# Optimization experiments

Hardware: AMD Instinct MI355X
Metric: run time of the kernel (lower is better)

## Reference

```python
import jax, jax.numpy as jnp
import numpy as np

D_MODEL = 768
N_LAYER = 4
VOCAB = 50280
D_STATE = 16
D_INNER = 1536
DT_RANK = 48
D_CONV = 4
BATCH = 2
SEQ = 1024
EPS = 1e-5


def setup_inputs() -> dict:
    key = jax.random.key(0)
    ks = jax.random.split(key, 8)
    s = 0.02
    A_log = jnp.broadcast_to(
        jnp.log(jnp.arange(1, D_STATE + 1, dtype=jnp.float32)),
        (N_LAYER, D_INNER, D_STATE)).copy()
    return {
        "input_ids": jax.random.randint(ks[0], (BATCH, SEQ), 0, VOCAB, dtype=jnp.int32),
        "embedding": jax.random.normal(ks[1], (VOCAB, D_MODEL)) * s,
        "in_proj_w": jax.random.normal(ks[2], (N_LAYER, D_MODEL, 2 * D_INNER)) * s,
        "conv_w": jax.random.normal(ks[3], (N_LAYER, D_INNER, D_CONV)) * s,
        "conv_b": jnp.zeros((N_LAYER, D_INNER)),
        "x_proj_w": jax.random.normal(ks[4], (N_LAYER, D_INNER, DT_RANK + 2 * D_STATE)) * s,
        "dt_proj_w": jax.random.normal(ks[5], (N_LAYER, DT_RANK, D_INNER)) * s,
        "dt_proj_b": jnp.zeros((N_LAYER, D_INNER)),
        "A_log": A_log,
        "D": jnp.ones((N_LAYER, D_INNER)),
        "out_proj_w": jax.random.normal(ks[6], (N_LAYER, D_INNER, D_MODEL)) * s,
        "norm_w": jnp.ones((N_LAYER, D_MODEL)),
        "norm_f_w": jnp.ones((D_MODEL,)),
    }


def rmsnorm(x, w):
    return x * jax.lax.rsqrt(jnp.mean(x * x, axis=-1, keepdims=True) + EPS) * w


def depthwise_causal_conv(x, w, b):
    # x: [b, l, d_in], w: [d_in, k] depthwise kernel, causal left padding (k-1)
    k = w.shape[-1]
    y = jax.lax.conv_general_dilated(
        x.transpose(0, 2, 1), w[:, None, :], window_strides=(1,),
        padding=[(k - 1, 0)], feature_group_count=w.shape[0],
        dimension_numbers=('NCH', 'OIH', 'NCH'))
    return y.transpose(0, 2, 1) + b


def selective_scan(u, delta, A, Bm, Cm, Dv):
    # u, delta: [b,l,d]; A: [d,n]; Bm,Cm: [b,l,n]; Dv: [d]
    deltaA = jnp.exp(delta[..., None] * A)                          # [b,l,d,n]
    deltaB_u = delta[..., None] * Bm[:, :, None, :] * u[..., None]  # [b,l,d,n]

    def step(x, inp):
        a_t, bu_t, c_t = inp            # [b,d,n], [b,d,n], [b,n]
        x = a_t * x + bu_t
        y = jnp.einsum('bdn,bn->bd', x, c_t)
        return x, y

    x0 = jnp.zeros((u.shape[0], u.shape[2], A.shape[1]), u.dtype)
    _, ys = jax.lax.scan(step, x0, (deltaA.transpose(1, 0, 2, 3),
                                    deltaB_u.transpose(1, 0, 2, 3),
                                    Cm.transpose(1, 0, 2)))
    return ys.transpose(1, 0, 2) + u * Dv


def mamba_block(x, in_w, cw, cb, xw, dtw, dtb, alog, d, ow):
    xr = x @ in_w                                   # [b,l,2*d_inner]
    xs, res = jnp.split(xr, 2, axis=-1)
    xs = jax.nn.silu(depthwise_causal_conv(xs, cw, cb))
    A = -jnp.exp(alog)
    xdbl = xs @ xw                                  # [b,l,dt_rank+2n]
    dlt = xdbl[..., :DT_RANK]
    Bm = xdbl[..., DT_RANK:DT_RANK + D_STATE]
    Cm = xdbl[..., DT_RANK + D_STATE:]
    dlt = jax.nn.softplus(dlt @ dtw + dtb)
    y = selective_scan(xs, dlt, A, Bm, Cm, d)
    return (y * jax.nn.silu(res)) @ ow


def reference(input_ids, embedding, in_proj_w, conv_w, conv_b, x_proj_w,
              dt_proj_w, dt_proj_b, A_log, D, out_proj_w, norm_w, norm_f_w):
    x = embedding[input_ids]                        # [b,l,d_model]

    def layer_step(x, p):
        in_w, cw, cb, xw, dtw, dtb, alog, d, ow, nw = p
        x = x + mamba_block(rmsnorm(x, nw), in_w, cw, cb, xw, dtw, dtb, alog, d, ow)
        return x, None

    x, _ = jax.lax.scan(layer_step, x,
                        (in_proj_w, conv_w, conv_b, x_proj_w, dt_proj_w,
                         dt_proj_b, A_log, D, out_proj_w, norm_w))
    x = rmsnorm(x, norm_f_w)
    return x @ embedding.T                          # tied lm_head: [b,l,vocab]
```

## Files before the change

kernel.cpp:

```cpp
#include <hip/hip_runtime.h>
#include <hip/hip_bf16.h>

typedef __hip_bfloat16 bf16;
typedef __attribute__((ext_vector_type(4))) float f32x4;
typedef __attribute__((ext_vector_type(8))) short s16x8;

#define D_MODEL 768
#define N_LAYER 4
#define VOCAB 50280
#define D_STATE 16
#define D_INNER 1536
#define DT_RANK 48
#define D_CONV 4
#define BATCH 2
#define SEQ 1024
#define NTOK (BATCH * SEQ)
#define NCHUNK 16
#define CHUNK (SEQ / NCHUNK)

static __device__ __forceinline__ float bf2f(bf16 v) { return __bfloat162float(v); }
static __device__ __forceinline__ int swz(int b) { return b ^ (((b >> 7) & 3) << 4); }

__global__ __launch_bounds__(256) void convert_f32_bf16_kernel(
    const float* __restrict__ in, bf16* __restrict__ out, long n4) {
  long i = (long)blockIdx.x * 256 + threadIdx.x;
  long stride = (long)gridDim.x * 256;
  for (; i < n4; i += stride) {
    float4 v = ((const float4*)in)[i];
    bf16 o[4] = {__float2bfloat16(v.x), __float2bfloat16(v.y),
                 __float2bfloat16(v.z), __float2bfloat16(v.w)};
    ((ushort4*)out)[i] = *(const ushort4*)o;
  }
}

__global__ __launch_bounds__(256) void transpose_f32_bf16_kernel(
    const float* __restrict__ in, bf16* __restrict__ out, int R, int C, int Rpad) {
  __shared__ float tile[32][33];
  const float* src = in + (size_t)blockIdx.z * R * C;
  bf16* dst = out + (size_t)blockIdx.z * C * Rpad;
  int c0 = blockIdx.x * 32, r0 = blockIdx.y * 32;
  int tx = threadIdx.x, ty = threadIdx.y;
  #pragma unroll
  for (int i = 0; i < 32; i += 8) {
    int r = r0 + ty + i, c = c0 + tx;
    if (c < C) tile[ty + i][tx] = (r < R) ? src[(size_t)r * C + c] : 0.f;
  }
  __syncthreads();
  #pragma unroll
  for (int i = 0; i < 32; i += 8) {
    int rr = c0 + ty + i, cc = r0 + tx;
    if (rr < C && cc < Rpad) dst[(size_t)rr * Rpad + cc] = __float2bfloat16(tile[tx][ty + i]);
  }
}

__global__ __launch_bounds__(256) void embed_kernel(
    const int* __restrict__ ids, const float* __restrict__ emb, float* __restrict__ x) {
  int m = blockIdx.x;
  int id = ids[m];
  const float* row = emb + (size_t)id * D_MODEL;
  for (int k = threadIdx.x; k < D_MODEL; k += 256)
    x[(size_t)m * D_MODEL + k] = row[k];
}

__global__ __launch_bounds__(256) void rmsnorm_kernel(
    const float* __restrict__ x, const float* __restrict__ w, bf16* __restrict__ out) {
  int m = blockIdx.x;
  const float* row = x + (size_t)m * D_MODEL;
  float ss = 0.f;
  for (int k = threadIdx.x; k < D_MODEL; k += 256) { float v = row[k]; ss = fmaf(v, v, ss); }
  #pragma unroll
  for (int msk = 32; msk >= 1; msk >>= 1) ss += __shfl_xor(ss, msk);
  __shared__ float part[4];
  __shared__ float scs;
  if ((threadIdx.x & 63) == 0) part[threadIdx.x >> 6] = ss;
  __syncthreads();
  if (threadIdx.x == 0) {
    float tot = part[0] + part[1] + part[2] + part[3];
    scs = rsqrtf(tot / (float)D_MODEL + 1e-5f);
  }
  __syncthreads();
  float scale = scs;
  for (int k = threadIdx.x; k < D_MODEL; k += 256)
    out[(size_t)m * D_MODEL + k] = __float2bfloat16(row[k] * scale * w[k]);
}

template <int EPI>
__global__ __launch_bounds__(256) void gemm128_kernel(
    const bf16* __restrict__ A, const bf16* __restrict__ BT,
    float* __restrict__ Cf, bf16* __restrict__ Cb, int M, int N, int K) {
  const int nm = M >> 7;
  const int total = gridDim.x;
  const int q = total >> 3, r = total & 7;
  int lin = blockIdx.x;
  int xcd = lin & 7, off = lin >> 3;
  int sw = (xcd < r ? xcd * (q + 1) : r * (q + 1) + (xcd - r) * q) + off;
  const int m0 = (sw % nm) * 128, n0 = (sw / nm) * 128;

  const int tid = threadIdx.x, lane = tid & 63, w = tid >> 6;
  const int wr = w >> 1, wc = w & 1;
  const int r16 = lane & 15, kc = lane >> 4;

  __shared__ __attribute__((aligned(16))) bf16 As[2][128 * 32];
  __shared__ __attribute__((aligned(16))) bf16 Bs[2][128 * 32];

  f32x4 acc[4][4];
  #pragma unroll
  for (int i = 0; i < 4; ++i)
    #pragma unroll
    for (int j = 0; j < 4; ++j) acc[i][j] = (f32x4){0.f, 0.f, 0.f, 0.f};

  auto stage = [&](int buf, int k0) {
    #pragma unroll
    for (int i = 0; i < 2; ++i) {
      int o = i * 4096 + w * 1024 + lane * 16;
      int row = o >> 6, cb = swz(o) & 63;
      const char* gA = (const char*)A + ((size_t)(m0 + row) * K + k0) * 2 + cb;
      int gn = n0 + row; if (gn > N - 1) gn = N - 1;
      const char* gB = (const char*)BT + ((size_t)gn * K + k0) * 2 + cb;
      __builtin_amdgcn_global_load_lds(
          (const __attribute__((address_space(1))) void*)gA,
          (__attribute__((address_space(3))) void*)((char*)As[buf] + i * 4096 + w * 1024), 16, 0, 0);
      __builtin_amdgcn_global_load_lds(
          (const __attribute__((address_space(1))) void*)gB,
          (__attribute__((address_space(3))) void*)((char*)Bs[buf] + i * 4096 + w * 1024), 16, 0, 0);
    }
  };

  const int nk = K >> 5;
  stage(0, 0);
  if (nk > 1) stage(1, 32);
  int cur = 0;
  for (int t = 0; t < nk; ++t) {
    if (t + 1 < nk) asm volatile("s_waitcnt vmcnt(4)" ::: "memory");
    else            asm volatile("s_waitcnt vmcnt(0)" ::: "memory");
    __builtin_amdgcn_s_barrier();

    s16x8 af[4], bfr[4];
    #pragma unroll
    for (int mi = 0; mi < 4; ++mi) {
      int row = wr * 64 + mi * 16 + r16;
      af[mi] = *(const s16x8*)((const char*)As[cur] + swz(row * 64 + kc * 16));
    }
    #pragma unroll
    for (int ni = 0; ni < 4; ++ni) {
      int row = wc * 64 + ni * 16 + r16;
      bfr[ni] = *(const s16x8*)((const char*)Bs[cur] + swz(row * 64 + kc * 16));
    }
    #pragma unroll
    for (int mi = 0; mi < 4; ++mi)
      #pragma unroll
      for (int ni = 0; ni < 4; ++ni)
        acc[mi][ni] = __builtin_amdgcn_mfma_f32_16x16x32_bf16(af[mi], bfr[ni], acc[mi][ni], 0, 0, 0);

    asm volatile("" ::: "memory");
    __builtin_amdgcn_s_barrier();
    if (t + 2 < nk) stage(cur, (t + 2) << 5);
    cur ^= 1;
  }

  #pragma unroll
  for (int mi = 0; mi < 4; ++mi) {
    #pragma unroll
    for (int ni = 0; ni < 4; ++ni) {
      int col = n0 + wc * 64 + ni * 16 + r16;
      if (col < N) {
        #pragma unroll
        for (int j = 0; j < 4; ++j) {
          int rowg = m0 + wr * 64 + mi * 16 + kc * 4 + j;
          size_t idx = (size_t)rowg * N + col;
          if (EPI == 0) Cf[idx] = acc[mi][ni][j];
          else Cb[idx] = __float2bfloat16(acc[mi][ni][j]);
        }
      }
    }
  }
}

template <int EPI>
__global__ __launch_bounds__(256) void gemm64_kernel(
    const bf16* __restrict__ A, const bf16* __restrict__ BT,
    float* __restrict__ Cf, const float* __restrict__ bias, int M, int N, int K) {
  const int nm = M >> 6;
  const int m0 = (blockIdx.x % nm) * 64, n0 = (blockIdx.x / nm) * 64;
  const int tid = threadIdx.x, lane = tid & 63, w = tid >> 6;
  const int wr = w >> 1, wc = w & 1;
  const int r16 = lane & 15, kc = lane >> 4;

  __shared__ __attribute__((aligned(16))) bf16 As[2][64 * 32];
  __shared__ __attribute__((aligned(16))) bf16 Bs[2][64 * 32];

  f32x4 acc[2][2];
  #pragma unroll
  for (int i = 0; i < 2; ++i)
    #pragma unroll
    for (int j = 0; j < 2; ++j) acc[i][j] = (f32x4){0.f, 0.f, 0.f, 0.f};

  auto stage = [&](int buf, int k0) {
    int o = tid * 16;
    int row = o >> 6, cb = swz(o) & 63;
    const char* gA = (const char*)A + ((size_t)(m0 + row) * K + k0) * 2 + cb;
    const char* gB = (const char*)BT + ((size_t)(n0 + row) * K + k0) * 2 + cb;
    __builtin_amdgcn_global_load_lds(
        (const __attribute__((address_space(1))) void*)gA,
        (__attribute__((address_space(3))) void*)((char*)As[buf] + w * 1024), 16, 0, 0);
    __builtin_amdgcn_global_load_lds(
        (const __attribute__((address_space(1))) void*)gB,
        (__attribute__((address_space(3))) void*)((char*)Bs[buf] + w * 1024), 16, 0, 0);
  };

  const int nk = K >> 5;
  stage(0, 0);
  __syncthreads();
  int cur = 0;
  for (int t = 0; t < nk; ++t) {
    if (t + 1 < nk) stage(cur ^ 1, (t + 1) << 5);
    s16x8 af[2], bfr[2];
    #pragma unroll
    for (int mi = 0; mi < 2; ++mi) {
      int row = wr * 32 + mi * 16 + r16;
      af[mi] = *(const s16x8*)((const char*)As[cur] + swz(row * 64 + kc * 16));
    }
    #pragma unroll
    for (int ni = 0; ni < 2; ++ni) {
      int row = wc * 32 + ni * 16 + r16;
      bfr[ni] = *(const s16x8*)((const char*)Bs[cur] + swz(row * 64 + kc * 16));
    }
    #pragma unroll
    for (int mi = 0; mi < 2; ++mi)
      #pragma unroll
      for (int ni = 0; ni < 2; ++ni)
        acc[mi][ni] = __builtin_amdgcn_mfma_f32_16x16x32_bf16(af[mi], bfr[ni], acc[mi][ni], 0, 0, 0);
    __syncthreads();
    cur ^= 1;
  }

  #pragma unroll
  for (int mi = 0; mi < 2; ++mi) {
    #pragma unroll
    for (int ni = 0; ni < 2; ++ni) {
      int col = n0 + wc * 32 + ni * 16 + r16;
      #pragma unroll
      for (int j = 0; j < 4; ++j) {
        int rowg = m0 + wr * 32 + mi * 16 + kc * 4 + j;
        size_t idx = (size_t)rowg * N + col;
        float v = acc[mi][ni][j];
        if (EPI == 1) Cf[idx] += v;
        else {
          float t = v + bias[col];
          Cf[idx] = (t > 20.f) ? t : log1pf(__expf(t));
        }
      }
    }
  }
}

__global__ __launch_bounds__(256) void conv_silu_kernel(
    const bf16* __restrict__ xzb, const float* __restrict__ cw, const float* __restrict__ cb,
    bf16* __restrict__ ubf) {
  int m = blockIdx.x;
  int d = blockIdx.y * 256 + threadIdx.x;
  int s = m & (SEQ - 1);
  float acc = cb[d];
  #pragma unroll
  for (int j = 0; j < D_CONV; ++j) {
    int sj = s - 3 + j;
    if (sj >= 0) acc += bf2f(xzb[(size_t)(m - 3 + j) * (2 * D_INNER) + d]) * cw[d * D_CONV + j];
  }
  float sv = acc / (1.f + __expf(-acc));
  ubf[(size_t)m * D_INNER + d] = __float2bfloat16(sv);
}

__global__ __launch_bounds__(256) void xproj_mfma_kernel(
    const bf16* __restrict__ ubf, const bf16* __restrict__ xpwT,
    float* __restrict__ xdbl, bf16* __restrict__ dltb) {
  const int m0 = blockIdx.x * 16;
  const int tid = threadIdx.x, lane = tid & 63, w = tid >> 6;
  const int r16 = lane & 15, kc = lane >> 4;
  __shared__ float part[4][16][80];

  f32x4 acc[5];
  #pragma unroll
  for (int ni = 0; ni < 5; ++ni) acc[ni] = (f32x4){0.f, 0.f, 0.f, 0.f};

  const char* aBase = (const char*)ubf + (size_t)(m0 + r16) * 3072;
  #pragma unroll 4
  for (int kk = 0; kk < 12; ++kk) {
    int koff = (w * 384 + kk * 32) * 2 + kc * 16;
    s16x8 a = *(const s16x8*)(aBase + koff);
    #pragma unroll
    for (int ni = 0; ni < 5; ++ni) {
      s16x8 b = *(const s16x8*)((const char*)xpwT + (size_t)(ni * 16 + r16) * 3072 + koff);
      acc[ni] = __builtin_amdgcn_mfma_f32_16x16x32_bf16(a, b, acc[ni], 0, 0, 0);
    }
  }
  #pragma unroll
  for (int ni = 0; ni < 5; ++ni)
    #pragma unroll
    for (int j = 0; j < 4; ++j)
      part[w][kc * 4 + j][ni * 16 + r16] = acc[ni][j];
  __syncthreads();

  for (int i = tid; i < 16 * 80; i += 256) {
    int row = i / 80, col = i - row * 80;
    float s = part[0][row][col] + part[1][row][col] +
              part[2][row][col] + part[3][row][col];
    xdbl[(size_t)(m0 + row) * 80 + col] = s;
    if (col < DT_RANK) dltb[(size_t)(m0 + row) * 64 + col] = __float2bfloat16(s);
  }
  {
    int row = tid >> 4, k = DT_RANK + (tid & 15);
    dltb[(size_t)(m0 + row) * 64 + k] = __float2bfloat16(0.f);
  }
}

template <int PASS>
__global__ __launch_bounds__(256) void scan_chunk_kernel(
    const float* __restrict__ delta, const bf16* __restrict__ ubf,
    const float* __restrict__ xdbl, const bf16* __restrict__ xzb,
    const float* __restrict__ A_log, const float* __restrict__ Dvec,
    float* __restrict__ Aprod, float* __restrict__ xpart,
    bf16* __restrict__ ybf) {
  int bd = blockIdx.x;
  int c = blockIdx.y;
  int b = bd / (D_INNER / 16), dblk = bd % (D_INNER / 16);
  int grp = threadIdx.x >> 4, n = threadIdx.x & 15;
  int d = dblk * 16 + grp;
  const size_t cstride = (size_t)BATCH * D_INNER * D_STATE;
  size_t si0 = ((size_t)b * D_INNER + d) * 16 + n;

  float Adn = -__expf(A_log[(size_t)d * D_STATE + n]);
  float Dd = Dvec[d];
  float xs = 0.f;
  if (PASS == 1) {
    for (int cc = 0; cc < c; ++cc)
      xs = fmaf(Aprod[cc * cstride + si0], xs, xpart[cc * cstride + si0]);
  }
  float ap = 1.f;
  size_t mbase = (size_t)b * SEQ + (size_t)c * CHUNK;
  #pragma unroll 4
  for (int t = 0; t < CHUNK; ++t) {
    size_t m = mbase + t;
    float dlt = delta[m * D_INNER + d];
    float uv = bf2f(ubf[m * D_INNER + d]);
    float Bv = xdbl[m * 80 + DT_RANK + n];
    float a = __expf(dlt * Adn);
    xs = fmaf(a, xs, dlt * Bv * uv);
    if (PASS == 0) {
      ap *= a;
    } else {
      float Cv = xdbl[m * 80 + DT_RANK + D_STATE + n];
      float p = xs * Cv;
      p += __shfl_xor(p, 1);
      p += __shfl_xor(p, 2);
      p += __shfl_xor(p, 4);
      p += __shfl_xor(p, 8);
      if (n == 0) {
        float rv = bf2f(xzb[m * (2 * D_INNER) + D_INNER + d]);
        float y = p + uv * Dd;
        float g = rv / (1.f + __expf(-rv));
        ybf[m * D_INNER + d] = __float2bfloat16(y * g);
      }
    }
  }
  if (PASS == 0) {
    Aprod[c * cstride + si0] = ap;
    xpart[c * cstride + si0] = xs;
  }
}

extern "C" void kernel_launch(void* const* d_in, const int* in_sizes, int n_in,
                              void* d_out, int out_size, void* d_ws, size_t ws_size,
                              hipStream_t stream) {
  const int* ids = (const int*)d_in[0];
  const float* emb = (const float*)d_in[1];
  const float* in_w = (const float*)d_in[2];
  const float* conv_w = (const float*)d_in[3];
  const float* conv_b = (const float*)d_in[4];
  const float* xp_w = (const float*)d_in[5];
  const float* dt_w = (const float*)d_in[6];
  const float* dt_b = (const float*)d_in[7];
  const float* A_log = (const float*)d_in[8];
  const float* Dv = (const float*)d_in[9];
  const float* out_w = (const float*)d_in[10];
  const float* norm_w = (const float*)d_in[11];
  const float* norm_f = (const float*)d_in[12];
  float* out = (float*)d_out;

  char* p = (char*)d_ws;
  auto alloc = [&](size_t bytes) {
    char* r = p;
    p += (bytes + 255) & ~(size_t)255;
    return r;
  };
  float* x    = (float*)alloc((size_t)NTOK * D_MODEL * 4);
  bf16*  h    = (bf16*)alloc((size_t)NTOK * D_MODEL * 2);
  bf16*  xn   = (bf16*)alloc((size_t)NTOK * D_MODEL * 2);
  bf16*  xzb  = (bf16*)alloc((size_t)NTOK * 2 * D_INNER * 2);
  bf16*  ubf  = (bf16*)alloc((size_t)NTOK * D_INNER * 2);
  float* xdbl = (float*)alloc((size_t)NTOK * 80 * 4);
  bf16*  dltb = (bf16*)alloc((size_t)NTOK * 64 * 2);
  float* delta= (float*)alloc((size_t)NTOK * D_INNER * 4);
  bf16*  ybf  = (bf16*)alloc((size_t)NTOK * D_INNER * 2);
  float* Aprod= (float*)alloc((size_t)NCHUNK * BATCH * D_INNER * D_STATE * 4);
  float* xpart= (float*)alloc((size_t)NCHUNK * BATCH * D_INNER * D_STATE * 4);
  bf16*  in_wT  = (bf16*)alloc((size_t)N_LAYER * 2 * D_INNER * D_MODEL * 2);
  bf16*  out_wT = (bf16*)alloc((size_t)N_LAYER * D_MODEL * D_INNER * 2);
  bf16*  xp_wT  = (bf16*)alloc((size_t)N_LAYER * 80 * D_INNER * 2);
  bf16*  dt_wT  = (bf16*)alloc((size_t)N_LAYER * D_INNER * 64 * 2);
  bf16*  emb_bf = (bf16*)alloc((size_t)VOCAB * D_MODEL * 2);

  dim3 tb(32, 8);
  convert_f32_bf16_kernel<<<2048, 256, 0, stream>>>(
      emb, emb_bf, (long)VOCAB * D_MODEL / 4);
  transpose_f32_bf16_kernel<<<dim3(3072 / 32, 768 / 32, N_LAYER), tb, 0, stream>>>(
      in_w, in_wT, D_MODEL, 2 * D_INNER, D_MODEL);
  transpose_f32_bf16_kernel<<<dim3(768 / 32, 1536 / 32, N_LAYER), tb, 0, stream>>>(
      out_w, out_wT, D_INNER, D_MODEL, D_INNER);
  transpose_f32_bf16_kernel<<<dim3(3, 1536 / 32, N_LAYER), tb, 0, stream>>>(
      xp_w, xp_wT, D_INNER, 80, D_INNER);
  transpose_f32_bf16_kernel<<<dim3(1536 / 32, 2, N_LAYER), tb, 0, stream>>>(
      dt_w, dt_wT, DT_RANK, D_INNER, 64);

  embed_kernel<<<NTOK, 256, 0, stream>>>(ids, emb, x);

  for (int l = 0; l < N_LAYER; ++l) {
    const bf16* inwT_l = in_wT + (size_t)l * 2 * D_INNER * D_MODEL;
    const bf16* outwT_l = out_wT + (size_t)l * D_MODEL * D_INNER;
    const bf16* xpwT_l = xp_wT + (size_t)l * 80 * D_INNER;
    const bf16* dtwT_l = dt_wT + (size_t)l * D_INNER * 64;
    const float* Al = A_log + (size_t)l * D_INNER * D_STATE;
    const float* Dl = Dv + (size_t)l * D_INNER;

    rmsnorm_kernel<<<NTOK, 256, 0, stream>>>(x, norm_w + (size_t)l * D_MODEL, h);

    gemm128_kernel<3><<<(NTOK / 128) * (2 * D_INNER / 128), 256, 0, stream>>>(
        h, inwT_l, nullptr, xzb, NTOK, 2 * D_INNER, D_MODEL);

    conv_silu_kernel<<<dim3(NTOK, D_INNER / 256), 256, 0, stream>>>(
        xzb, conv_w + (size_t)l * D_INNER * D_CONV, conv_b + (size_t)l * D_INNER, ubf);

    xproj_mfma_kernel<<<NTOK / 16, 256, 0, stream>>>(ubf, xpwT_l, xdbl, dltb);

    gemm64_kernel<2><<<(NTOK / 64) * (D_INNER / 64), 256, 0, stream>>>(
        dltb, dtwT_l, delta, dt_b + (size_t)l * D_INNER, NTOK, D_INNER, 64);

    dim3 sgrid(BATCH * (D_INNER / 16), NCHUNK);
    scan_chunk_kernel<0><<<sgrid, 256, 0, stream>>>(
        delta, ubf, xdbl, xzb, Al, Dl, Aprod, xpart, nullptr);
    scan_chunk_kernel<1><<<sgrid, 256, 0, stream>>>(
        delta, ubf, xdbl, xzb, Al, Dl, Aprod, xpart, ybf);

    gemm64_kernel<1><<<(NTOK / 64) * (D_MODEL / 64), 256, 0, stream>>>(
        ybf, outwT_l, x, nullptr, NTOK, D_MODEL, D_INNER);
  }

  rmsnorm_kernel<<<NTOK, 256, 0, stream>>>(x, norm_f, xn);

  gemm128_kernel<0><<<(NTOK / 128) * ((VOCAB + 127) / 128), 256, 0, stream>>>(
      xn, emb_bf, out, nullptr, NTOK, VOCAB, D_MODEL);
}
```

Before: 1.228 ms.

## Fuse RMSNorm into in_proj GEMM and conv/x_proj/dt_proj into one kernel

```diff
diff --git a/kernel.cpp b/kernel.cpp
--- a/kernel.cpp
+++ b/kernel.cpp
@@ -84,10 +84,125 @@
     out[(size_t)m * D_MODEL + k] = __float2bfloat16(row[k] * scale * w[k]);
 }
 
-template <int EPI>
+__global__ __launch_bounds__(256) void inproj_rms_kernel(
+    const float* __restrict__ X, const float* __restrict__ nw,
+    const bf16* __restrict__ BT, bf16* __restrict__ Cb, int M, int N, int K) {
+  const int nm = M >> 7;
+  const int m0 = (blockIdx.x % nm) * 128, n0 = (blockIdx.x / nm) * 128;
+  const int tid = threadIdx.x, lane = tid & 63, w = tid >> 6;
+  const int wr = w >> 1, wc = w & 1;
+  const int r16 = lane & 15, kc = lane >> 4;
+
+  __shared__ __attribute__((aligned(16))) bf16 As[2][128 * 32];
+  __shared__ __attribute__((aligned(16))) bf16 Bs[2][128 * 32];
+  __shared__ float nws[768];
+  __shared__ float scl[128];
+
+  for (int i = tid; i < 768; i += 256) nws[i] = nw[i];
+  for (int rr = 0; rr < 32; ++rr) {
+    int row = w * 32 + rr;
+    const float* rp = X + (size_t)(m0 + row) * 768 + lane * 12;
+    float ss = 0.f;
+    #pragma unroll
+    for (int j = 0; j < 3; ++j) {
+      float4 v = *(const float4*)(rp + j * 4);
+      ss += v.x * v.x + v.y * v.y + v.z * v.z + v.w * v.w;
+    }
+    #pragma unroll
+    for (int msk = 32; msk >= 1; msk >>= 1) ss += __shfl_xor(ss, msk);
+    if (lane == 0) scl[row] = rsqrtf(ss / 768.f + 1e-5f);
+  }
+  __syncthreads();
+
+  const int arow = tid >> 1, acg = tid & 1;
+  float4 av[4];
+  auto loadA = [&](int k0) {
+    const float* ap = X + (size_t)(m0 + arow) * 768 + k0 + acg * 16;
+    #pragma unroll
+    for (int j = 0; j < 4; ++j) av[j] = *(const float4*)(ap + j * 4);
+  };
+  auto writeA = [&](int buf, int k0) {
+    float s = scl[arow];
+    int kb = k0 + acg * 16;
+    bf16 tmp[16];
+    #pragma unroll
+    for (int j = 0; j < 4; ++j) {
+      tmp[j * 4 + 0] = __float2bfloat16(av[j].x * s * nws[kb + j * 4 + 0]);
+      tmp[j * 4 + 1] = __float2bfloat16(av[j].y * s * nws[kb + j * 4 + 1]);
+      tmp[j * 4 + 2] = __float2bfloat16(av[j].z * s * nws[kb + j * 4 + 2]);
+      tmp[j * 4 + 3] = __float2bfloat16(av[j].w * s * nws[kb + j * 4 + 3]);
+    }
+    #pragma unroll
+    for (int g = 0; g < 2; ++g) {
+      int o = arow * 64 + acg * 32 + g * 16;
+      *(s16x8*)((char*)As[buf] + swz(o)) = *(const s16x8*)(tmp + g * 8);
+    }
+  };
+  auto stageB = [&](int buf, int k0) {
+    #pragma unroll
+    for (int i = 0; i < 2; ++i) {
+      int o = i * 4096 + w * 1024 + lane * 16;
+      int row = o >> 6, cb2 = swz(o) & 63;
+      const char* gB = (const char*)BT + ((size_t)(n0 + row) * K + k0) * 2 + cb2;
+      __builtin_amdgcn_global_load_lds(
+          (const __attribute__((address_space(1))) void*)gB,
+          (__attribute__((address_space(3))) void*)((char*)Bs[buf] + i * 4096 + w * 1024), 16, 0, 0);
+    }
+  };
+
+  f32x4 acc[4][4];
+  #pragma unroll
+  for (int i = 0; i < 4; ++i)
+    #pragma unroll
+    for (int j = 0; j < 4; ++j) acc[i][j] = (f32x4){0.f, 0.f, 0.f, 0.f};
+
+  const int nk = K >> 5;
+  loadA(0); stageB(0, 0);
+  writeA(0, 0);
+  __syncthreads();
+  int cur = 0;
+  for (int t = 0; t < nk; ++t) {
+    s16x8 af[4], bfr[4];
+    #pragma unroll
+    for (int mi = 0; mi < 4; ++mi) {
+      int row = wr * 64 + mi * 16 + r16;
+      af[mi] = *(const s16x8*)((const char*)As[cur] + swz(row * 64 + kc * 16));
+    }
+    #pragma unroll
+    for (int ni = 0; ni < 4; ++ni) {
+      int row = wc * 64 + ni * 16 + r16;
+      bfr[ni] = *(const s16x8*)((const char*)Bs[cur] + swz(row * 64 + kc * 16));
+    }
+    if (t + 1 < nk) { stageB(cur ^ 1, (t + 1) << 5); loadA((t + 1) << 5); }
+    #pragma unroll
+    for (int mi = 0; mi < 4; ++mi)
+      #pragma unroll
+      for (int ni = 0; ni < 4; ++ni)
+        acc[mi][ni] = __builtin_amdgcn_mfma_f32_16x16x32_bf16(af[mi], bfr[ni], acc[mi][ni], 0, 0, 0);
+    if (t + 1 < nk) writeA(cur ^ 1, (t + 1) << 5);
+    __syncthreads();
+    cur ^= 1;
+  }
+
+  #pragma unroll
+  for (int mi = 0; mi < 4; ++mi) {
+    #pragma unroll
+    for (int ni = 0; ni < 4; ++ni) {
+      int col = n0 + wc * 64 + ni * 16 + r16;
+      if (col < N) {
+        #pragma unroll
+        for (int j = 0; j < 4; ++j) {
+          int rowg = m0 + wr * 64 + mi * 16 + kc * 4 + j;
+          Cb[(size_t)rowg * N + col] = __float2bfloat16(acc[mi][ni][j]);
+        }
+      }
+    }
+  }
+}
+
 __global__ __launch_bounds__(256) void gemm128_kernel(
     const bf16* __restrict__ A, const bf16* __restrict__ BT,
-    float* __restrict__ Cf, bf16* __restrict__ Cb, int M, int N, int K) {
+    float* __restrict__ Cf, int M, int N, int K) {
   const int nm = M >> 7;
   const int total = gridDim.x;
   const int q = total >> 3, r = total & 7;
@@ -167,19 +282,16 @@
         #pragma unroll
         for (int j = 0; j < 4; ++j) {
           int rowg = m0 + wr * 64 + mi * 16 + kc * 4 + j;
-          size_t idx = (size_t)rowg * N + col;
-          if (EPI == 0) Cf[idx] = acc[mi][ni][j];
-          else Cb[idx] = __float2bfloat16(acc[mi][ni][j]);
+          Cf[(size_t)rowg * N + col] = acc[mi][ni][j];
         }
       }
     }
   }
 }
 
-template <int EPI>
-__global__ __launch_bounds__(256) void gemm64_kernel(
+__global__ __launch_bounds__(256) void gemm64_acc_kernel(
     const bf16* __restrict__ A, const bf16* __restrict__ BT,
-    float* __restrict__ Cf, const float* __restrict__ bias, int M, int N, int K) {
+    float* __restrict__ Cf, int M, int N, int K) {
   const int nm = M >> 6;
   const int m0 = (blockIdx.x % nm) * 64, n0 = (blockIdx.x / nm) * 64;
   const int tid = threadIdx.x, lane = tid & 63, w = tid >> 6;
@@ -242,74 +354,87 @@
       #pragma unroll
       for (int j = 0; j < 4; ++j) {
         int rowg = m0 + wr * 32 + mi * 16 + kc * 4 + j;
-        size_t idx = (size_t)rowg * N + col;
-        float v = acc[mi][ni][j];
-        if (EPI == 1) Cf[idx] += v;
-        else {
-          float t = v + bias[col];
-          Cf[idx] = (t > 20.f) ? t : log1pf(__expf(t));
-        }
+        Cf[(size_t)rowg * N + col] += acc[mi][ni][j];
       }
     }
   }
 }
 
-__global__ __launch_bounds__(256) void conv_silu_kernel(
+__global__ __launch_bounds__(256) void fused_mid2_kernel(
     const bf16* __restrict__ xzb, const float* __restrict__ cw, const float* __restrict__ cb,
-    bf16* __restrict__ ubf) {
-  int m = blockIdx.x;
-  int d = blockIdx.y * 256 + threadIdx.x;
-  int s = m & (SEQ - 1);
-  float acc = cb[d];
-  #pragma unroll
-  for (int j = 0; j < D_CONV; ++j) {
-    int sj = s - 3 + j;
-    if (sj >= 0) acc += bf2f(xzb[(size_t)(m - 3 + j) * (2 * D_INNER) + d]) * cw[d * D_CONV + j];
-  }
-  float sv = acc / (1.f + __expf(-acc));
-  ubf[(size_t)m * D_INNER + d] = __float2bfloat16(sv);
-}
-
-__global__ __launch_bounds__(256) void xproj_mfma_kernel(
-    const bf16* __restrict__ ubf, const bf16* __restrict__ xpwT,
-    float* __restrict__ xdbl, bf16* __restrict__ dltb) {
-  const int m0 = blockIdx.x * 16;
+    const bf16* __restrict__ xpwT, const float* __restrict__ dtw, const float* __restrict__ dtb,
+    bf16* __restrict__ ubf, float* __restrict__ xdbl, float* __restrict__ delta) {
+  const int m0 = blockIdx.x * 8;
   const int tid = threadIdx.x, lane = tid & 63, w = tid >> 6;
   const int r16 = lane & 15, kc = lane >> 4;
-  __shared__ float part[4][16][80];
-
-  f32x4 acc[5];
-  #pragma unroll
-  for (int ni = 0; ni < 5; ++ni) acc[ni] = (f32x4){0.f, 0.f, 0.f, 0.f};
-
-  const char* aBase = (const char*)ubf + (size_t)(m0 + r16) * 3072;
+  __shared__ __attribute__((aligned(16))) char usb[8 * 3072];
+  __shared__ float part[4][8][80];
+  __shared__ float dl[8][DT_RANK];
+
+  for (int tok = 0; tok < 8; ++tok) {
+    int m = m0 + tok, s = m & (SEQ - 1);
+    for (int d = tid; d < D_INNER; d += 256) {
+      float acc = cb[d];
+      #pragma unroll
+      for (int j = 0; j < D_CONV; ++j) {
+        int sj = s - 3 + j;
+        if (sj >= 0) acc += bf2f(xzb[(size_t)(m - 3 + j) * (2 * D_INNER) + d]) * cw[d * D_CONV + j];
+      }
+      float sv = acc / (1.f + __expf(-acc));
+      bf16 hv = __float2bfloat16(sv);
+      ubf[(size_t)m * D_INNER + d] = hv;
+      *(bf16*)(usb + tok * 3072 + ((d * 2) ^ ((tok & 7) << 4))) = hv;
+    }
+  }
+  __syncthreads();
+
+  f32x4 acc5[5];
+  #pragma unroll
+  for (int ni = 0; ni < 5; ++ni) acc5[ni] = (f32x4){0.f, 0.f, 0.f, 0.f};
+  const int trow = r16 & 7;
   #pragma unroll 4
   for (int kk = 0; kk < 12; ++kk) {
     int koff = (w * 384 + kk * 32) * 2 + kc * 16;
-    s16x8 a = *(const s16x8*)(aBase + koff);
+    s16x8 a = *(const s16x8*)(usb + trow * 3072 + (koff ^ (trow << 4)));
     #pragma unroll
     for (int ni = 0; ni < 5; ++ni) {
       s16x8 b = *(const s16x8*)((const char*)xpwT + (size_t)(ni * 16 + r16) * 3072 + koff);
-      acc[ni] = __builtin_amdgcn_mfma_f32_16x16x32_bf16(a, b, acc[ni], 0, 0, 0);
-    }
-  }
-  #pragma unroll
-  for (int ni = 0; ni < 5; ++ni)
-    #pragma unroll
-    for (int j = 0; j < 4; ++j)
-      part[w][kc * 4 + j][ni * 16 + r16] = acc[ni][j];
-  __syncthreads();
-
-  for (int i = tid; i < 16 * 80; i += 256) {
+      acc5[ni] = __builtin_amdgcn_mfma_f32_16x16x32_bf16(a, b, acc5[ni], 0, 0, 0);
+    }
+  }
+  if (kc < 2) {
+    #pragma unroll
+    for (int ni = 0; ni < 5; ++ni)
+      #pragma unroll
+      for (int j = 0; j < 4; ++j)
+        part[w][kc * 4 + j][ni * 16 + r16] = acc5[ni][j];
+  }
+  __syncthreads();
+
+  for (int i = tid; i < 8 * 80; i += 256) {
     int row = i / 80, col = i - row * 80;
     float s = part[0][row][col] + part[1][row][col] +
               part[2][row][col] + part[3][row][col];
     xdbl[(size_t)(m0 + row) * 80 + col] = s;
-    if (col < DT_RANK) dltb[(size_t)(m0 + row) * 64 + col] = __float2bfloat16(s);
-  }
-  {
-    int row = tid >> 4, k = DT_RANK + (tid & 15);
-    dltb[(size_t)(m0 + row) * 64 + k] = __float2bfloat16(0.f);
+    if (col < DT_RANK) dl[row][col] = s;
+  }
+  __syncthreads();
+
+  for (int d = tid; d < D_INNER; d += 256) {
+    float a8[8];
+    float bias = dtb[d];
+    #pragma unroll
+    for (int t = 0; t < 8; ++t) a8[t] = bias;
+    for (int r = 0; r < DT_RANK; ++r) {
+      float wv = dtw[(size_t)r * D_INNER + d];
+      #pragma unroll
+      for (int t = 0; t < 8; ++t) a8[t] = fmaf(dl[t][r], wv, a8[t]);
+    }
+    #pragma unroll
+    for (int t = 0; t < 8; ++t) {
+      float v = a8[t];
+      delta[(size_t)(m0 + t) * D_INNER + d] = (v > 20.f) ? v : log1pf(__expf(v));
+    }
   }
 }
 
@@ -393,12 +518,10 @@
     return r;
   };
   float* x    = (float*)alloc((size_t)NTOK * D_MODEL * 4);
-  bf16*  h    = (bf16*)alloc((size_t)NTOK * D_MODEL * 2);
   bf16*  xn   = (bf16*)alloc((size_t)NTOK * D_MODEL * 2);
   bf16*  xzb  = (bf16*)alloc((size_t)NTOK * 2 * D_INNER * 2);
   bf16*  ubf  = (bf16*)alloc((size_t)NTOK * D_INNER * 2);
   float* xdbl = (float*)alloc((size_t)NTOK * 80 * 4);
-  bf16*  dltb = (bf16*)alloc((size_t)NTOK * 64 * 2);
   float* delta= (float*)alloc((size_t)NTOK * D_INNER * 4);
   bf16*  ybf  = (bf16*)alloc((size_t)NTOK * D_INNER * 2);
   float* Aprod= (float*)alloc((size_t)NCHUNK * BATCH * D_INNER * D_STATE * 4);
@@ -406,7 +529,6 @@
   bf16*  in_wT  = (bf16*)alloc((size_t)N_LAYER * 2 * D_INNER * D_MODEL * 2);
   bf16*  out_wT = (bf16*)alloc((size_t)N_LAYER * D_MODEL * D_INNER * 2);
   bf16*  xp_wT  = (bf16*)alloc((size_t)N_LAYER * 80 * D_INNER * 2);
-  bf16*  dt_wT  = (bf16*)alloc((size_t)N_LAYER * D_INNER * 64 * 2);
   bf16*  emb_bf = (bf16*)alloc((size_t)VOCAB * D_MODEL * 2);
 
   dim3 tb(32, 8);
@@ -418,8 +540,6 @@
       out_w, out_wT, D_INNER, D_MODEL, D_INNER);
   transpose_f32_bf16_kernel<<<dim3(3, 1536 / 32, N_LAYER), tb, 0, stream>>>(
       xp_w, xp_wT, D_INNER, 80, D_INNER);
-  transpose_f32_bf16_kernel<<<dim3(1536 / 32, 2, N_LAYER), tb, 0, stream>>>(
-      dt_w, dt_wT, DT_RANK, D_INNER, 64);
 
   embed_kernel<<<NTOK, 256, 0, stream>>>(ids, emb, x);
 
@@ -427,22 +547,16 @@
     const bf16* inwT_l = in_wT + (size_t)l * 2 * D_INNER * D_MODEL;
     const bf16* outwT_l = out_wT + (size_t)l * D_MODEL * D_INNER;
     const bf16* xpwT_l = xp_wT + (size_t)l * 80 * D_INNER;
-    const bf16* dtwT_l = dt_wT + (size_t)l * D_INNER * 64;
     const float* Al = A_log + (size_t)l * D_INNER * D_STATE;
     const float* Dl = Dv + (size_t)l * D_INNER;
 
-    rmsnorm_kernel<<<NTOK, 256, 0, stream>>>(x, norm_w + (size_t)l * D_MODEL, h);
-
-    gemm128_kernel<3><<<(NTOK / 128) * (2 * D_INNER / 128), 256, 0, stream>>>(
-        h, inwT_l, nullptr, xzb, NTOK, 2 * D_INNER, D_MODEL);
-
-    conv_silu_kernel<<<dim3(NTOK, D_INNER / 256), 256, 0, stream>>>(
-        xzb, conv_w + (size_t)l * D_INNER * D_CONV, conv_b + (size_t)l * D_INNER, ubf);
-
-    xproj_mfma_kernel<<<NTOK / 16, 256, 0, stream>>>(ubf, xpwT_l, xdbl, dltb);
-
-    gemm64_kernel<2><<<(NTOK / 64) * (D_INNER / 64), 256, 0, stream>>>(
-        dltb, dtwT_l, delta, dt_b + (size_t)l * D_INNER, NTOK, D_INNER, 64);
+    inproj_rms_kernel<<<(NTOK / 128) * (2 * D_INNER / 128), 256, 0, stream>>>(
+        x, norm_w + (size_t)l * D_MODEL, inwT_l, xzb, NTOK, 2 * D_INNER, D_MODEL);
+
+    fused_mid2_kernel<<<NTOK / 8, 256, 0, stream>>>(
+        xzb, conv_w + (size_t)l * D_INNER * D_CONV, conv_b + (size_t)l * D_INNER,
+        xpwT_l, dt_w + (size_t)l * DT_RANK * D_INNER, dt_b + (size_t)l * D_INNER,
+        ubf, xdbl, delta);
 
     dim3 sgrid(BATCH * (D_INNER / 16), NCHUNK);
     scan_chunk_kernel<0><<<sgrid, 256, 0, stream>>>(
@@ -450,12 +564,12 @@
     scan_chunk_kernel<1><<<sgrid, 256, 0, stream>>>(
         delta, ubf, xdbl, xzb, Al, Dl, Aprod, xpart, ybf);
 
-    gemm64_kernel<1><<<(NTOK / 64) * (D_MODEL / 64), 256, 0, stream>>>(
-        ybf, outwT_l, x, nullptr, NTOK, D_MODEL, D_INNER);
+    gemm64_acc_kernel<<<(NTOK / 64) * (D_MODEL / 64), 256, 0, stream>>>(
+        ybf, outwT_l, x, NTOK, D_MODEL, D_INNER);
   }
 
   rmsnorm_kernel<<<NTOK, 256, 0, stream>>>(x, norm_f, xn);
 
-  gemm128_kernel<0><<<(NTOK / 128) * ((VOCAB + 127) / 128), 256, 0, stream>>>(
-      xn, emb_bf, out, nullptr, NTOK, VOCAB, D_MODEL);
-}
+  gemm128_kernel<<<(NTOK / 128) * ((VOCAB + 127) / 128), 256, 0, stream>>>(
+      xn, emb_bf, out, NTOK, VOCAB, D_MODEL);
+}
```

New measurement: 1.473 ms. 1.2x slower.
